# Kernel tuning notes

Hardware: AMD Instinct MI355X
Metric: run time of the kernel (lower is better)

Reference implementation:

```python
import jax, jax.numpy as jnp
import numpy as np

N_NODES = 100000
N_EDGES = 1600000
IN_CH = 64
OUT_CH = 64


def setup_inputs() -> dict:
    key = jax.random.key(0)
    k1, k2, k3, k4, k5, k6 = jax.random.split(key, 6)
    x = jax.random.normal(k1, (N_NODES, IN_CH), dtype=jnp.float32)
    edge_index = jax.random.randint(k2, (2, N_EDGES), 0, N_NODES, dtype=jnp.int64)
    edge_attr = jax.random.uniform(k3, (N_EDGES, 3), dtype=jnp.float32)
    root_weight = jax.random.normal(k4, (IN_CH, OUT_CH), dtype=jnp.float32)
    bias = jax.random.normal(k5, (OUT_CH,), dtype=jnp.float32)
    gaussian_param = jnp.ones((1,), dtype=jnp.float32)
    return {"x": x, "edge_index": edge_index, "edge_attr": edge_attr,
            "root_weight": root_weight, "bias": bias,
            "gaussian_param": gaussian_param}


def reference(x, edge_index, edge_attr, root_weight, bias, gaussian_param):
    src = edge_index[0]
    tgt = edge_index[1]
    # per-edge gaussian weight from distance (edge_attr[:, 0])
    dist = edge_attr[:, 0:1]                                  # [E, 1]
    gw = jnp.exp(-dist ** 2 / (gaussian_param ** 2 + 1e-8))   # [E, 1]
    # gather -> matmul -> scale
    messages = (x[src] @ root_weight) * gw                    # [E, out]
    # scatter-add to target nodes
    out = jax.ops.segment_sum(messages, tgt, num_segments=x.shape[0])
    out = out + x @ root_weight + bias
    return out
```

## Files before the change

kernel.cpp:

```cpp
#include <hip/hip_runtime.h>
#include <hip/hip_bf16.h>
#include <stdint.h>

#define N_NODES 100000
#define N_EDGES 1600000
#define CH 64

#define NPB 128
#define NBUCK ((N_NODES + NPB - 1) / NPB)
#define CHUNK 4096
#define BT 1024
#define EPT (CHUNK / BT)
#define NBLK_E ((N_EDGES + CHUNK - 1) / CHUNK)

#define STRIDE 2560
#define CAP 3072
#define ST 512

#define GM 64

typedef float f32x4 __attribute__((ext_vector_type(4)));

__device__ __forceinline__ unsigned short bf16rn(float f) {
  unsigned u = __float_as_uint(f);
  unsigned r = u + 0x7FFFu + ((u >> 16) & 1u);
  return (unsigned short)(r >> 16);
}


__global__ __launch_bounds__(BT) void bin2_kernel(const int* __restrict__ ei,
                                                  const float* __restrict__ attr,
                                                  const float* __restrict__ gp,
                                                  int* __restrict__ gcur,
                                                  uint2* __restrict__ recs,
                                                  const float* __restrict__ x,
                                                  unsigned short* __restrict__ xh) {
  __shared__ int lhist[NBUCK];
  __shared__ int lbase[NBUCK];
  const int tid = threadIdx.x;
  for (int i = tid; i < NBUCK; i += BT) lhist[i] = 0;
  __syncthreads();
  const int cbase = blockIdx.x * CHUNK;
  const float inv = 1.0f / (gp[0] * gp[0] + 1e-8f);

  int s[EPT], t[EPT], lrank[EPT];
  float g[EPT];
#pragma unroll
  for (int k = 0; k < EPT; ++k) {
    const int e = cbase + k * BT + tid;
    if (e < N_EDGES) {
      s[k] = ei[e];
      t[k] = ei[N_EDGES + e];
      const float d = attr[3 * e];
      g[k] = __expf(-d * d * inv);
      lrank[k] = atomicAdd(&lhist[t[k] >> 7], 1);
    }
  }
  {
    const int nq = N_NODES * CH / 4;
    const int stride = gridDim.x * BT;
    for (int q = blockIdx.x * BT + tid; q < nq; q += stride) {
      const float4 v = reinterpret_cast<const float4*>(x)[q];
      ushort4 o;
      o.x = bf16rn(v.x);
      o.y = bf16rn(v.y);
      o.z = bf16rn(v.z);
      o.w = bf16rn(v.w);
      reinterpret_cast<ushort4*>(xh)[q] = o;
    }
  }
  __syncthreads();
  for (int i = tid; i < NBUCK; i += BT) {
    const int c = lhist[i];
    if (c) lbase[i] = i * STRIDE + atomicAdd(&gcur[i], c);
  }
  __syncthreads();

#pragma unroll
  for (int k = 0; k < EPT; ++k) {
    const int e = cbase + k * BT + tid;
    if (e < N_EDGES) {
      const int bb = t[k] >> 7;
      const int idx = lbase[bb] + lrank[k];
      if (idx < (bb + 1) * STRIDE) {
        uint2 rec;
        rec.x = (unsigned)s[k] | ((unsigned)(t[k] & (NPB - 1)) << 17);
        rec.y = __float_as_uint(g[k]);
        recs[idx] = rec;
      }
    }
  }
}

__global__ __launch_bounds__(ST) void sortb2_kernel(const int* __restrict__ gcur,
                                                    uint2* __restrict__ recs,
                                                    int* __restrict__ offs,
                                                    int* __restrict__ ends) {
  __shared__ uint2 srec[STRIDE];
  __shared__ int lhist[NPB];
  __shared__ int lofs[NPB];
  __shared__ int lcur[NPB];
  const int b = blockIdx.x;
  const int tid = threadIdx.x;
  const int start = b * STRIDE;
  int cnt = gcur[b];
  cnt = cnt < STRIDE ? cnt : STRIDE;

  if (tid < NPB) lhist[tid] = 0;
  __syncthreads();
  for (int i = tid; i < cnt; i += ST) {
    const uint2 r = recs[start + i];
    srec[i] = r;
    atomicAdd(&lhist[r.x >> 17], 1);
  }
  __syncthreads();
  if (tid < NPB) lofs[tid] = lhist[tid];
  __syncthreads();
  for (int off = 1; off < NPB; off <<= 1) {
    int t = 0;
    if (tid < NPB && tid >= off) t = lofs[tid - off];
    __syncthreads();
    if (tid < NPB) lofs[tid] += t;
    __syncthreads();
  }
  if (tid < NPB) {
    const int incl = lofs[tid];
    const int excl = incl - lhist[tid];
    lcur[tid] = excl;
    const int node = b * NPB + tid;
    if (node < N_NODES) {
      offs[node] = start + excl;
      ends[node] = start + incl;
    }
  }
  __syncthreads();
  for (int i = tid; i < cnt; i += ST) {
    const uint2 r = srec[i];
    const int pos = atomicAdd(&lcur[r.x >> 17], 1);
    recs[start + pos] = r;
  }
}


__global__ __launch_bounds__(BT) void hist2_kernel(const int* __restrict__ ei,
                                                   int* __restrict__ ghist,
                                                   const float* __restrict__ x,
                                                   unsigned short* __restrict__ xh,
                                                   int do_conv) {
  __shared__ int lh[NBUCK];
  const int tid = threadIdx.x;
  for (int i = tid; i < NBUCK; i += BT) lh[i] = 0;
  __syncthreads();
  const int cbase = blockIdx.x * CHUNK;
#pragma unroll
  for (int k = 0; k < EPT; ++k) {
    const int e = cbase + k * BT + tid;
    if (e < N_EDGES) atomicAdd(&lh[ei[N_EDGES + e] >> 7], 1);
  }
  if (do_conv) {
    const int nq = N_NODES * CH / 4;
    const int stride = gridDim.x * BT;
    for (int q = blockIdx.x * BT + tid; q < nq; q += stride) {
      const float4 v = reinterpret_cast<const float4*>(x)[q];
      ushort4 o;
      o.x = bf16rn(v.x);
      o.y = bf16rn(v.y);
      o.z = bf16rn(v.z);
      o.w = bf16rn(v.w);
      reinterpret_cast<ushort4*>(xh)[q] = o;
    }
  }
  __syncthreads();
  for (int i = tid; i < NBUCK; i += BT) {
    const int c = lh[i];
    if (c) atomicAdd(&ghist[i], c);
  }
}

__global__ __launch_bounds__(1024) void scan_kernel(const int* __restrict__ ghist,
                                                    int* __restrict__ gbase,
                                                    int* __restrict__ gcur) {
  __shared__ int sd[1024];
  const int tid = threadIdx.x;
  const int v = (tid < NBUCK) ? ghist[tid] : 0;
  sd[tid] = v;
  __syncthreads();
  for (int off = 1; off < 1024; off <<= 1) {
    int t = (tid >= off) ? sd[tid - off] : 0;
    __syncthreads();
    sd[tid] += t;
    __syncthreads();
  }
  if (tid < NBUCK) {
    const int excl = sd[tid] - v;
    gbase[tid] = excl;
    gcur[tid] = excl;
  }
}

__global__ __launch_bounds__(BT) void bin_kernel(const int* __restrict__ ei,
                                                 const float* __restrict__ attr,
                                                 const float* __restrict__ gp,
                                                 int* __restrict__ gcur,
                                                 uint2* __restrict__ recs) {
  __shared__ int lhist[NBUCK];
  __shared__ int lbase[NBUCK];
  const int tid = threadIdx.x;
  for (int i = tid; i < NBUCK; i += BT) lhist[i] = 0;
  __syncthreads();
  const int cbase = blockIdx.x * CHUNK;
  const float inv = 1.0f / (gp[0] * gp[0] + 1e-8f);

  int s[EPT], t[EPT], lrank[EPT];
  float g[EPT];
#pragma unroll
  for (int k = 0; k < EPT; ++k) {
    const int e = cbase + k * BT + tid;
    if (e < N_EDGES) {
      s[k] = ei[e];
      t[k] = ei[N_EDGES + e];
      const float d = attr[3 * e];
      g[k] = __expf(-d * d * inv);
      lrank[k] = atomicAdd(&lhist[t[k] >> 7], 1);
    }
  }
  __syncthreads();
  for (int i = tid; i < NBUCK; i += BT) {
    const int c = lhist[i];
    if (c) lbase[i] = atomicAdd(&gcur[i], c);
  }
  __syncthreads();

#pragma unroll
  for (int k = 0; k < EPT; ++k) {
    const int e = cbase + k * BT + tid;
    if (e < N_EDGES) {
      uint2 rec;
      rec.x = (unsigned)s[k] | ((unsigned)(t[k] & (NPB - 1)) << 17);
      rec.y = __float_as_uint(g[k]);
      recs[lbase[t[k] >> 7] + lrank[k]] = rec;
    }
  }
}

__global__ __launch_bounds__(ST) void sortb_kernel(const int* __restrict__ gbase,
                                                   const int* __restrict__ ghist,
                                                   uint2* __restrict__ recs,
                                                   int* __restrict__ offs) {
  __shared__ uint2 srec[CAP];
  __shared__ int lhist[NPB];
  __shared__ int lofs[NPB];
  __shared__ int lcur[NPB];
  const int b = blockIdx.x;
  const int tid = threadIdx.x;
  const int start = gbase[b];
  const int cnt = ghist[b] < CAP ? ghist[b] : CAP;

  if (tid < NPB) lhist[tid] = 0;
  __syncthreads();
  for (int i = tid; i < cnt; i += ST) {
    const uint2 r = recs[start + i];
    srec[i] = r;
    atomicAdd(&lhist[r.x >> 17], 1);
  }
  __syncthreads();
  if (tid < NPB) lofs[tid] = lhist[tid];
  __syncthreads();
  for (int off = 1; off < NPB; off <<= 1) {
    int t = 0;
    if (tid < NPB && tid >= off) t = lofs[tid - off];
    __syncthreads();
    if (tid < NPB) lofs[tid] += t;
    __syncthreads();
  }
  if (tid < NPB) {
    const int excl = lofs[tid] - lhist[tid];
    lcur[tid] = excl;
    const int node = b * NPB + tid;
    if (node < N_NODES) offs[node] = start + excl;
  }
  if (b == NBUCK - 1 && tid == 0) offs[N_NODES] = start + cnt;
  __syncthreads();
  for (int i = tid; i < cnt; i += ST) {
    const uint2 r = srec[i];
    const int pos = atomicAdd(&lcur[r.x >> 17], 1);
    recs[start + pos] = r;
  }
}


__global__ __launch_bounds__(256) void reduce7h_kernel(
    const float* __restrict__ x, const unsigned short* __restrict__ xh,
    const int* __restrict__ offs, const int* __restrict__ ends,
    const uint2* __restrict__ recs, float* __restrict__ out) {
  const int node = (blockIdx.x * blockDim.x + threadIdx.x) >> 6;
  if (node >= N_NODES) return;
  const int lane = threadIdx.x & 63;
  const int c2 = lane & 31;
  const int eh = lane >> 5;
  const int n0 = __builtin_amdgcn_readfirstlane(offs[node]);
  const int n1 = __builtin_amdgcn_readfirstlane(ends[node]);
  const int m = n1 - n0;

  float ax = 0.0f, ay = 0.0f;
  int j = 0;
  for (; j + 16 <= m; j += 16) {
#pragma unroll
    for (int p = 0; p < 8; ++p) {
      const uint2 r0 = recs[n0 + j + 2 * p];
      const uint2 r1 = recs[n0 + j + 2 * p + 1];
      const unsigned sx = (eh ? r1.x : r0.x) & 0x1FFFFu;
      const float g = __uint_as_float(eh ? r1.y : r0.y);
      const unsigned u =
          *reinterpret_cast<const unsigned*>(&xh[(size_t)sx * CH + c2 * 2]);
      ax += g * __uint_as_float(u << 16);
      ay += g * __uint_as_float(u & 0xFFFF0000u);
    }
  }
  for (; j + 8 <= m; j += 8) {
#pragma unroll
    for (int p = 0; p < 4; ++p) {
      const uint2 r0 = recs[n0 + j + 2 * p];
      const uint2 r1 = recs[n0 + j + 2 * p + 1];
      const unsigned sx = (eh ? r1.x : r0.x) & 0x1FFFFu;
      const float g = __uint_as_float(eh ? r1.y : r0.y);
      const unsigned u =
          *reinterpret_cast<const unsigned*>(&xh[(size_t)sx * CH + c2 * 2]);
      ax += g * __uint_as_float(u << 16);
      ay += g * __uint_as_float(u & 0xFFFF0000u);
    }
  }
  for (; j < m; j += 2) {
    const uint2 r0 = recs[n0 + j];
    uint2 r1 = {0u, 0u};
    if (j + 1 < m) r1 = recs[n0 + j + 1];
    const unsigned sx = (eh ? r1.x : r0.x) & 0x1FFFFu;
    const float g = __uint_as_float(eh ? r1.y : r0.y);
    const unsigned u =
        *reinterpret_cast<const unsigned*>(&xh[(size_t)sx * CH + c2 * 2]);
    ax += g * __uint_as_float(u << 16);
    ay += g * __uint_as_float(u & 0xFFFF0000u);
  }
  ax += __shfl_xor(ax, 32);
  ay += __shfl_xor(ay, 32);
  if (lane < 32) {
    const float2 xv =
        reinterpret_cast<const float2*>(x + (size_t)node * CH)[c2];
    float2 o;
    o.x = ax + xv.x;
    o.y = ay + xv.y;
    reinterpret_cast<float2*>(out + (size_t)node * CH)[c2] = o;
  }
}

__global__ __launch_bounds__(256) void reduce3_kernel(
    const float* __restrict__ x, const int* __restrict__ offs,
    const uint2* __restrict__ recs, float* __restrict__ out) {
  const int node = (blockIdx.x * blockDim.x + threadIdx.x) >> 6;
  if (node >= N_NODES) return;
  const int lane = threadIdx.x & 63;
  const int n0 = offs[node];
  const int m = offs[node + 1] - n0;

  float acc = 0.0f;
  for (int base = 0; base < m; base += 64) {
    const int mm = (m - base) < 64 ? (m - base) : 64;
    uint2 pr = {0u, 0u};
    if (lane < mm) pr = recs[n0 + base + lane];
    const int pk_all = (int)pr.x;
    const float g_all = __uint_as_float(pr.y);
    int j = 0;
    for (; j + 4 <= mm; j += 4) {
      const int s0 = __shfl(pk_all, j + 0) & 0x1FFFF;
      const int s1 = __shfl(pk_all, j + 1) & 0x1FFFF;
      const int s2 = __shfl(pk_all, j + 2) & 0x1FFFF;
      const int s3 = __shfl(pk_all, j + 3) & 0x1FFFF;
      const float g0 = __shfl(g_all, j + 0);
      const float g1 = __shfl(g_all, j + 1);
      const float g2 = __shfl(g_all, j + 2);
      const float g3 = __shfl(g_all, j + 3);
      acc += g0 * x[(size_t)s0 * CH + lane] + g1 * x[(size_t)s1 * CH + lane] +
             g2 * x[(size_t)s2 * CH + lane] + g3 * x[(size_t)s3 * CH + lane];
    }
    for (; j < mm; ++j) {
      const int sj = __shfl(pk_all, j) & 0x1FFFF;
      const float gj = __shfl(g_all, j);
      acc += gj * x[(size_t)sj * CH + lane];
    }
  }
  out[(size_t)node * CH + lane] = acc + x[(size_t)node * CH + lane];
}

__global__ __launch_bounds__(256) void scatter_kernel(
    const float* __restrict__ x, const int* __restrict__ ei,
    const float* __restrict__ attr, const float* __restrict__ gp,
    float* __restrict__ agg) {
  const int lane = threadIdx.x & 63;
  const int wave = (blockIdx.x * blockDim.x + threadIdx.x) >> 6;
  const int nwaves = (gridDim.x * blockDim.x) >> 6;
  const float inv = 1.0f / (gp[0] * gp[0] + 1e-8f);
  for (int base = wave * 64; base < N_EDGES; base += nwaves * 64) {
    const int e = base + lane;
    const int s = ei[e];
    const int t = ei[N_EDGES + e];
    const float d = attr[3 * e];
    const float g = __expf(-d * d * inv);
#pragma unroll 1
    for (int j = 0; j < 64; ++j) {
      const int sj = __shfl(s, j);
      const int tj = __shfl(t, j);
      const float gj = __shfl(g, j);
      atomicAdd(&agg[(size_t)tj * CH + lane], gj * x[sj * CH + lane]);
    }
  }
}

__global__ __launch_bounds__(256) void rowgemm3_kernel(
    const float* __restrict__ W, const float* __restrict__ bias,
    float* __restrict__ out) {
  __shared__ float sT[64][GM + 4];
  __shared__ float wl[64 * 64];
  const int tid = threadIdx.x;
  const int node0 = blockIdx.x * GM;

  {
    const float4* W4 = reinterpret_cast<const float4*>(W);
    float4* wl4 = reinterpret_cast<float4*>(wl);
#pragma unroll
    for (int i = 0; i < 4; ++i) wl4[i * 256 + tid] = W4[i * 256 + tid];
  }
  {
    const int m = tid >> 2;
    const int kq = tid & 3;
    if (node0 + m < N_NODES) {
      const float4* r4 =
          reinterpret_cast<const float4*>(out + (size_t)(node0 + m) * CH);
#pragma unroll
      for (int q = 0; q < 4; ++q) {
        const float4 v = r4[kq * 4 + q];
        const int k = kq * 16 + q * 4;
        sT[k + 0][m] = v.x;
        sT[k + 1][m] = v.y;
        sT[k + 2][m] = v.z;
        sT[k + 3][m] = v.w;
      }
    }
  }
  __syncthreads();

  const int m0 = (tid >> 4) * 4;
  const int c0 = (tid & 15) * 4;

  const f32x4 b4 = *reinterpret_cast<const f32x4*>(&bias[c0]);
  f32x4 acc0 = b4, acc1 = b4, acc2 = b4, acc3 = b4;

#pragma unroll 8
  for (int k = 0; k < 64; ++k) {
    const f32x4 sv = *reinterpret_cast<const f32x4*>(&sT[k][m0]);
    const f32x4 wv = *reinterpret_cast<const f32x4*>(&wl[k * 64 + c0]);
    acc0 += sv.x * wv;
    acc1 += sv.y * wv;
    acc2 += sv.z * wv;
    acc3 += sv.w * wv;
  }

  __syncthreads();
  f32x4 accs[4] = {acc0, acc1, acc2, acc3};
#pragma unroll
  for (int i = 0; i < 4; ++i) {
    const int node = node0 + m0 + i;
    if (node < N_NODES)
      *reinterpret_cast<f32x4*>(&out[(size_t)node * CH + c0]) = accs[i];
  }
}

__global__ __launch_bounds__(256) void rowgemm_kernel(
    const float* __restrict__ x, const float* __restrict__ W,
    const float* __restrict__ bias, float* __restrict__ out) {
  const int r = blockIdx.x * blockDim.x + threadIdx.x;
  if (r >= N_NODES) return;
  const float* xr = x + (size_t)r * CH;
  float* outr = out + (size_t)r * CH;

  float s[CH];
#pragma unroll
  for (int k4 = 0; k4 < CH / 4; ++k4) {
    float4 xv = *reinterpret_cast<const float4*>(xr + k4 * 4);
    float4 av = *reinterpret_cast<const float4*>(outr + k4 * 4);
    s[k4 * 4 + 0] = xv.x + av.x;
    s[k4 * 4 + 1] = xv.y + av.y;
    s[k4 * 4 + 2] = xv.z + av.z;
    s[k4 * 4 + 3] = xv.w + av.w;
  }

  float acc[CH];
#pragma unroll
  for (int c = 0; c < CH; ++c) acc[c] = bias[c];

#pragma unroll
  for (int k = 0; k < CH; ++k) {
    const float sk = s[k];
#pragma unroll
    for (int c4 = 0; c4 < CH / 4; ++c4) {
      const float4 w = *reinterpret_cast<const float4*>(&W[k * CH + c4 * 4]);
      acc[c4 * 4 + 0] += sk * w.x;
      acc[c4 * 4 + 1] += sk * w.y;
      acc[c4 * 4 + 2] += sk * w.z;
      acc[c4 * 4 + 3] += sk * w.w;
    }
  }

#pragma unroll
  for (int c4 = 0; c4 < CH / 4; ++c4) {
    float4 o = {acc[c4 * 4 + 0], acc[c4 * 4 + 1], acc[c4 * 4 + 2],
                acc[c4 * 4 + 3]};
    *reinterpret_cast<float4*>(outr + c4 * 4) = o;
  }
}

extern "C" void kernel_launch(void* const* d_in, const int* in_sizes, int n_in,
                              void* d_out, int out_size, void* d_ws,
                              size_t ws_size, hipStream_t stream) {
  const float* x = (const float*)d_in[0];
  const int* ei = (const int*)d_in[1];
  const float* attr = (const float*)d_in[2];
  const float* W = (const float*)d_in[3];
  const float* bias = (const float*)d_in[4];
  const float* gp = (const float*)d_in[5];
  float* out = (float*)d_out;

  const size_t sz_i = ((size_t)NBUCK * 4 + 255) & ~(size_t)255;
  const size_t sz_xh = (size_t)N_NODES * CH * 2;
  const size_t sz_offs1 = ((size_t)N_NODES * 4 + 255) & ~(size_t)255;

  const size_t sz_recsA = (size_t)NBUCK * STRIDE * 8;
  const size_t need_fs = sz_i + sz_recsA + 2 * sz_offs1 + sz_xh;

  const size_t sz_recsB = (size_t)N_EDGES * 8;
  const size_t sz_offsB = ((size_t)(N_NODES + 1) * 4 + 255) & ~(size_t)255;
  const size_t need_b = 3 * sz_i + sz_recsB + sz_offsB;
  const size_t need_a = need_b + sz_xh;

  if (ws_size >= need_fs) {
    char* base = (char*)d_ws;
    int* gcur = (int*)base;
    uint2* recs = (uint2*)(base + sz_i);
    int* offs = (int*)(base + sz_i + sz_recsA);
    int* ends = (int*)(base + sz_i + sz_recsA + sz_offs1);
    unsigned short* xh =
        (unsigned short*)(base + sz_i + sz_recsA + 2 * sz_offs1);

    hipMemsetAsync(gcur, 0, (size_t)NBUCK * 4, stream);
    bin2_kernel<<<NBLK_E, BT, 0, stream>>>(ei, attr, gp, gcur, recs, x, xh);
    sortb2_kernel<<<NBUCK, ST, 0, stream>>>(gcur, recs, offs, ends);
    reduce7h_kernel<<<(N_NODES * 64 + 255) / 256, 256, 0, stream>>>(
        x, xh, offs, ends, recs, out);
    rowgemm3_kernel<<<(N_NODES + GM - 1) / GM, 256, 0, stream>>>(W, bias, out);
  } else if (ws_size >= need_b) {
    char* base = (char*)d_ws;
    int* ghist = (int*)base;
    int* gbase = (int*)(base + sz_i);
    int* gcur = (int*)(base + 2 * sz_i);
    uint2* recs = (uint2*)(base + 3 * sz_i);
    int* offs = (int*)(base + 3 * sz_i + sz_recsB);
    unsigned short* xh = (unsigned short*)(base + need_b);

    const int tier_a = (ws_size >= need_a) ? 1 : 0;
    hipMemsetAsync(ghist, 0, (size_t)NBUCK * 4, stream);
    hist2_kernel<<<NBLK_E, BT, 0, stream>>>(ei, ghist, x, xh, tier_a);
    scan_kernel<<<1, 1024, 0, stream>>>(ghist, gbase, gcur);
    bin_kernel<<<NBLK_E, BT, 0, stream>>>(ei, attr, gp, gcur, recs);
    sortb_kernel<<<NBUCK, ST, 0, stream>>>(gbase, ghist, recs, offs);
    if (tier_a)
      reduce7h_kernel<<<(N_NODES * 64 + 255) / 256, 256, 0, stream>>>(
          x, xh, offs, offs + 1, recs, out);
    else
      reduce3_kernel<<<(N_NODES * 64 + 255) / 256, 256, 0, stream>>>(x, offs,
                                                                     recs, out);
    rowgemm3_kernel<<<(N_NODES + GM - 1) / GM, 256, 0, stream>>>(W, bias, out);
  } else {
    hipMemsetAsync(out, 0, (size_t)N_NODES * CH * sizeof(float), stream);
    scatter_kernel<<<2048, 256, 0, stream>>>(x, ei, attr, gp, out);
    rowgemm_kernel<<<(N_NODES + 255) / 256, 256, 0, stream>>>(x, W, bias, out);
  }
}
```

Baseline: 107.7 us.

## Fuse dense root-weight matmul and bias into the gather-reduce kernel

Merges the separate row GEMM into the per-node reduce kernel. Each 1024-thread block loads W and the bias into shared memory, and each wavefront multiplies its aggregated 64-wide row by W using readlane broadcasts. This removes a kernel launch and a full write-then-read round trip of the output array. In exchange, every block reloads the 16KB W, and the per-node matmul runs scalar FMAs fed by readlanes instead of a tiled GEMM.

New measurement: 110.7 us. +2.8%, slower.

```diff
diff --git a/kernel.cpp b/kernel.cpp
--- a/kernel.cpp
+++ b/kernel.cpp
@@ -18,6 +18,7 @@
 #define ST 512
 
 #define GM 64
+#define NPBLK 16
 
 typedef float f32x4 __attribute__((ext_vector_type(4)));
 
@@ -25,6 +26,10 @@
   unsigned u = __float_as_uint(f);
   unsigned r = u + 0x7FFFu + ((u >> 16) & 1u);
   return (unsigned short)(r >> 16);
+}
+
+__device__ __forceinline__ float rdlane(float v, int l) {
+  return __uint_as_float(__builtin_amdgcn_readlane(__float_as_uint(v), l));
 }
 
 
@@ -289,13 +294,25 @@
 }
 
 
-__global__ __launch_bounds__(256) void reduce7h_kernel(
+__global__ __launch_bounds__(1024) void reduce8h_kernel(
     const float* __restrict__ x, const unsigned short* __restrict__ xh,
     const int* __restrict__ offs, const int* __restrict__ ends,
-    const uint2* __restrict__ recs, float* __restrict__ out) {
-  const int node = (blockIdx.x * blockDim.x + threadIdx.x) >> 6;
+    const uint2* __restrict__ recs, const float* __restrict__ W,
+    const float* __restrict__ bias, float* __restrict__ out) {
+  __shared__ float wl[CH * CH];
+  __shared__ float bl[CH];
+  const int tid = threadIdx.x;
+  {
+    const float4* W4 = reinterpret_cast<const float4*>(W);
+    float4* wl4 = reinterpret_cast<float4*>(wl);
+    wl4[tid] = W4[tid];
+    if (tid < CH) bl[tid] = bias[tid];
+  }
+  __syncthreads();
+
+  const int node = blockIdx.x * NPBLK + (tid >> 6);
   if (node >= N_NODES) return;
-  const int lane = threadIdx.x & 63;
+  const int lane = tid & 63;
   const int c2 = lane & 31;
   const int eh = lane >> 5;
   const int n0 = __builtin_amdgcn_readfirstlane(offs[node]);
@@ -343,14 +360,23 @@
   }
   ax += __shfl_xor(ax, 32);
   ay += __shfl_xor(ay, 32);
-  if (lane < 32) {
-    const float2 xv =
-        reinterpret_cast<const float2*>(x + (size_t)node * CH)[c2];
-    float2 o;
-    o.x = ax + xv.x;
-    o.y = ay + xv.y;
-    reinterpret_cast<float2*>(out + (size_t)node * CH)[c2] = o;
-  }
+  const float2 xv = reinterpret_cast<const float2*>(x + (size_t)node * CH)[c2];
+  ax += xv.x;
+  ay += xv.y;
+
+  float a0 = 0.f, a1 = 0.f, a2 = 0.f, a3 = 0.f;
+#pragma unroll
+  for (int k4 = 0; k4 < CH / 4; ++k4) {
+    const float s0 = rdlane(ax, 2 * k4);
+    const float s1 = rdlane(ay, 2 * k4);
+    const float s2 = rdlane(ax, 2 * k4 + 1);
+    const float s3 = rdlane(ay, 2 * k4 + 1);
+    a0 += s0 * wl[(4 * k4 + 0) * CH + lane];
+    a1 += s1 * wl[(4 * k4 + 1) * CH + lane];
+    a2 += s2 * wl[(4 * k4 + 2) * CH + lane];
+    a3 += s3 * wl[(4 * k4 + 3) * CH + lane];
+  }
+  out[(size_t)node * CH + lane] = bl[lane] + ((a0 + a1) + (a2 + a3));
 }
 
 __global__ __launch_bounds__(256) void reduce3_kernel(
@@ -553,9 +579,8 @@
     hipMemsetAsync(gcur, 0, (size_t)NBUCK * 4, stream);
     bin2_kernel<<<NBLK_E, BT, 0, stream>>>(ei, attr, gp, gcur, recs, x, xh);
     sortb2_kernel<<<NBUCK, ST, 0, stream>>>(gcur, recs, offs, ends);
-    reduce7h_kernel<<<(N_NODES * 64 + 255) / 256, 256, 0, stream>>>(
-        x, xh, offs, ends, recs, out);
-    rowgemm3_kernel<<<(N_NODES + GM - 1) / GM, 256, 0, stream>>>(W, bias, out);
+    reduce8h_kernel<<<(N_NODES + NPBLK - 1) / NPBLK, 1024, 0, stream>>>(
+        x, xh, offs, ends, recs, W, bias, out);
   } else if (ws_size >= need_b) {
     char* base = (char*)d_ws;
     int* ghist = (int*)base;
@@ -571,13 +596,15 @@
     scan_kernel<<<1, 1024, 0, stream>>>(ghist, gbase, gcur);
     bin_kernel<<<NBLK_E, BT, 0, stream>>>(ei, attr, gp, gcur, recs);
     sortb_kernel<<<NBUCK, ST, 0, stream>>>(gbase, ghist, recs, offs);
-    if (tier_a)
-      reduce7h_kernel<<<(N_NODES * 64 + 255) / 256, 256, 0, stream>>>(
-          x, xh, offs, offs + 1, recs, out);
-    else
+    if (tier_a) {
+      reduce8h_kernel<<<(N_NODES + NPBLK - 1) / NPBLK, 1024, 0, stream>>>(
+          x, xh, offs, offs + 1, recs, W, bias, out);
+    } else {
       reduce3_kernel<<<(N_NODES * 64 + 255) / 256, 256, 0, stream>>>(x, offs,
                                                                      recs, out);
-    rowgemm3_kernel<<<(N_NODES + GM - 1) / GM, 256, 0, stream>>>(W, bias, out);
+      rowgemm3_kernel<<<(N_NODES + GM - 1) / GM, 256, 0, stream>>>(W, bias,
+                                                                   out);
+    }
   } else {
     hipMemsetAsync(out, 0, (size_t)N_NODES * CH * sizeof(float), stream);
     scatter_kernel<<<2048, 256, 0, stream>>>(x, ei, attr, gp, out);
```
